# Kernel tuning notes

Measured on AMD Instinct MI355X. Metric: run time of the kernel, lower is better.

The kernel has to match this reference:

```python
import jax, jax.numpy as jnp
import numpy as np

D_MODEL = 1024
NUM_HEADS = 16
HEAD_DIM = D_MODEL // NUM_HEADS


def setup_inputs() -> dict:
    key = jax.random.key(0)
    k1, k2, k3, k4, k5 = jax.random.split(key, 5)
    s = 1.0 / np.sqrt(D_MODEL)
    return {
        "x": jax.random.normal(k1, (4, 2048, D_MODEL), dtype=jnp.float32),
        "Wqkv": jax.random.normal(k2, (D_MODEL, 3 * D_MODEL), dtype=jnp.float32) * s,
        "bqkv": jax.random.normal(k3, (3 * D_MODEL,), dtype=jnp.float32) * 0.01,
        "Wout": jax.random.normal(k4, (D_MODEL, D_MODEL), dtype=jnp.float32) * s,
        "bout": jax.random.normal(k5, (D_MODEL,), dtype=jnp.float32) * 0.01,
    }


def reference(x, Wqkv, bqkv, Wout, bout):
    B, S, _ = x.shape
    qkv = x @ Wqkv + bqkv                                   # [B, S, 3*D]
    qkv = qkv.reshape(B, S, NUM_HEADS, 3 * HEAD_DIM)
    qkv = jnp.transpose(qkv, (0, 2, 1, 3))                  # [B, H, S, 3*hd]
    q, k, v = jnp.split(qkv, 3, axis=-1)                    # each [B, H, S, hd]
    scale = 1.0 / jnp.sqrt(jnp.asarray(HEAD_DIM, dtype=x.dtype))
    scores = jnp.einsum("bhqd,bhkd->bhqk", q, k) * scale    # [B, H, S, S]
    attn = jax.nn.softmax(scores, axis=-1)
    out = jnp.einsum("bhqk,bhkd->bhqd", attn, v)            # [B, H, S, hd]
    out = jnp.transpose(out, (0, 2, 1, 3)).reshape(B, S, D_MODEL)
    return out @ Wout + bout
```

## Files before the change

### kernel.cpp

```cpp
#include <hip/hip_runtime.h>
#include <hip/hip_bf16.h>


#define S_ 2048
#define DM 1024
#define NH 16
#define HD 64

typedef unsigned short u16;
typedef unsigned int u32;
typedef __attribute__((ext_vector_type(8))) short short8;
typedef __attribute__((ext_vector_type(4))) float f32x4;
typedef __attribute__((ext_vector_type(16))) float f32x16;
typedef __attribute__((ext_vector_type(4))) u32 u32x4;

extern "C" __device__ float __ocml_native_exp2_f32(float);

#define MFMA(a, b, c) __builtin_amdgcn_mfma_f32_16x16x32_bf16((a), (b), (c), 0, 0, 0)
#define MFMA32(a, b, c) __builtin_amdgcn_mfma_f32_32x32x16_bf16((a), (b), (c), 0, 0, 0)
#define C1 0.18033688f

static __device__ __forceinline__ u16 f2bf(float f) {
  return __builtin_bit_cast(u16, __float2bfloat16(f));
}
static __device__ __forceinline__ u32 pack2bf(float a, float b) {
  return (u32)f2bf(a) | ((u32)f2bf(b) << 16);
}
static __device__ __forceinline__ short8 ld8(const u16* p) {
  return *reinterpret_cast<const short8*>(p);
}
static __device__ __forceinline__ void gl_lds16(const u16* g, u16* l) {
  __builtin_amdgcn_global_load_lds((__attribute__((address_space(1))) void*)(u16*)g,
                                   (__attribute__((address_space(3))) void*)l, 16, 0, 0);
}
static __device__ __forceinline__ void plswap(u32& a, u32& b) {
#if __has_builtin(__builtin_amdgcn_permlane32_swap)
  typedef __attribute__((ext_vector_type(2))) unsigned int u32x2_t;
  u32x2_t r = __builtin_amdgcn_permlane32_swap(a, b, false, false);
  a = r.x; b = r.y;
#else
  asm("v_permlane32_swap_b32 %0, %1" : "+v"(a), "+v"(b));
#endif
}
static __device__ __forceinline__ float xhalf_max(float x) {
  u32 a = __builtin_bit_cast(u32, x), b = a;
  plswap(a, b);
  return fmaxf(__builtin_bit_cast(float, a), __builtin_bit_cast(float, b));
}
static __device__ __forceinline__ float xhalf_sum(float x) {
  u32 a = __builtin_bit_cast(u32, x), b = a;
  plswap(a, b);
  return __builtin_bit_cast(float, a) + __builtin_bit_cast(float, b);
}

__global__ __launch_bounds__(256) void cast_x_kernel(const float4* __restrict__ in,
                                                     uint2* __restrict__ out, int n4) {
  int i = blockIdx.x * 256 + threadIdx.x;
  if (i >= n4) return;
  float4 v = in[i];
  uint2 o;
  o.x = pack2bf(v.x, v.y);
  o.y = pack2bf(v.z, v.w);
  out[i] = o;
}

__global__ __launch_bounds__(256) void transpose_cast_kernel(const float* __restrict__ in,
                                                             u16* __restrict__ out, int N) {
  __shared__ float tile[32][33];
  const int bk = blockIdx.y * 32, bn = blockIdx.x * 32;
  const int r = threadIdx.x >> 3, c4 = (threadIdx.x & 7) * 4;
  float4 v = *reinterpret_cast<const float4*>(&in[(size_t)(bk + r) * N + bn + c4]);
  tile[r][c4 + 0] = v.x; tile[r][c4 + 1] = v.y;
  tile[r][c4 + 2] = v.z; tile[r][c4 + 3] = v.w;
  __syncthreads();
  uint2 o;
  o.x = pack2bf(tile[c4 + 0][r], tile[c4 + 1][r]);
  o.y = pack2bf(tile[c4 + 2][r], tile[c4 + 3][r]);
  *reinterpret_cast<uint2*>(&out[(size_t)(bn + r) * 1024 + bk + c4]) = o;
}

__global__ __launch_bounds__(256) void gemm_bt_kernel(
    const u16* __restrict__ A, const u16* __restrict__ BT, const float* __restrict__ bias,
    int mode, u16* __restrict__ Qb, u16* __restrict__ Kb, u16* __restrict__ VT,
    float* __restrict__ outF) {
  __shared__ __align__(16) u16 As[128 * 32];
  __shared__ __align__(16) u16 Bs[128 * 32];
  const int tid = threadIdx.x, lane = tid & 63, wid = tid >> 6;
  const int m0 = blockIdx.y * 128, n0 = blockIdx.x * 128;
  const int wm = (wid >> 1) * 64, wn = (wid & 1) * 64;
  const int g = lane >> 4, lr = lane & 15;
  const int srow16 = lane >> 2, scol8 = (lane & 3) * 8;
  f32x4 acc[4][4] = {};

  for (int k0 = 0; k0 < 1024; k0 += 32) {
#pragma unroll
    for (int i = 0; i < 2; ++i) {
      int sA = wid + i * 4;
      gl_lds16(&A[(size_t)(m0 + sA * 16 + srow16) * 1024 + k0 + scol8], &As[sA * 512]);
      gl_lds16(&BT[(size_t)(n0 + sA * 16 + srow16) * 1024 + k0 + scol8], &Bs[sA * 512]);
    }
    __syncthreads();
    short8 af[4], bfr[4];
#pragma unroll
    for (int mb = 0; mb < 4; ++mb)
      af[mb] = ld8(&As[(wm + mb * 16 + lr) * 32 + g * 8]);
#pragma unroll
    for (int nb = 0; nb < 4; ++nb)
      bfr[nb] = ld8(&Bs[(wn + nb * 16 + lr) * 32 + g * 8]);
#pragma unroll
    for (int mb = 0; mb < 4; ++mb)
#pragma unroll
      for (int nb = 0; nb < 4; ++nb)
        acc[mb][nb] = MFMA(af[mb], bfr[nb], acc[mb][nb]);
    __syncthreads();
  }

  if (mode == 0) {
#pragma unroll
    for (int nb = 0; nb < 4; ++nb) {
      int col = n0 + wn + nb * 16 + lr;
      int hh = col / 192;
      int c = col - hh * 192;
      int t = c >> 6, d = c & 63;
      float bv = bias[col];
#pragma unroll
      for (int mb = 0; mb < 4; ++mb)
#pragma unroll
        for (int r = 0; r < 4; ++r) {
          int rowg = m0 + wm + mb * 16 + g * 4 + r;
          int b = rowg >> 11, s = rowg & 2047;
          u16 v = f2bf(acc[mb][nb][r] + bv);
          int head = b * NH + hh;
          if (t == 0)      Qb[(head * S_ + s) * HD + d] = v;
          else if (t == 1) Kb[(head * S_ + s) * HD + d] = v;
          else             VT[((size_t)head * HD + d) * S_ + s] = v;
        }
    }
  } else {
#pragma unroll
    for (int nb = 0; nb < 4; ++nb) {
      int col = n0 + wn + nb * 16 + lr;
      float bv = bias[col];
#pragma unroll
      for (int mb = 0; mb < 4; ++mb)
#pragma unroll
        for (int r = 0; r < 4; ++r) {
          int rowg = m0 + wm + mb * 16 + g * 4 + r;
          outF[(size_t)rowg * DM + col] = acc[mb][nb][r] + bv;
        }
    }
  }
}

__global__ __launch_bounds__(256, 2) void attn_kernel(const u16* __restrict__ Qb,
                                                      const u16* __restrict__ Kb,
                                                      const u16* __restrict__ VT,
                                                      u16* __restrict__ attn_out) {
  const int lane = threadIdx.x & 63, wid = threadIdx.x >> 6;
  const int i = blockIdx.x;
  const int head = ((i >> 7) << 3) | (i & 7);
  const int qb = (i >> 3) & 15;
  const int l31 = lane & 31, hi = lane >> 5;
  const int q = qb * 128 + wid * 32 + l31;
  const u16* Qh = Qb + (size_t)head * S_ * HD;
  const u16* Kh = Kb + (size_t)head * S_ * HD;
  const u16* Vh = VT + (size_t)head * HD * S_;

  short8 qf[4];
#pragma unroll
  for (int dt = 0; dt < 4; ++dt)
    qf[dt] = ld8(&Qh[q * HD + dt * 16 + hi * 8]);

  short8 kf[2][4];
#pragma unroll
  for (int kt = 0; kt < 2; ++kt)
#pragma unroll
    for (int dt = 0; dt < 4; ++dt)
      kf[kt][dt] = ld8(&Kh[(kt * 32 + l31) * HD + dt * 16 + hi * 8]);

  f32x16 o0 = {}, o1 = {};
  float m_run = -1e30f, l_run = 0.f;

#pragma unroll 1
  for (int kv0 = 0; kv0 < S_; kv0 += 64) {
    short8 vf0[4], vf1[4];
#pragma unroll
    for (int kc = 0; kc < 4; ++kc) {
      vf0[kc] = ld8(&Vh[(size_t)l31 * S_ + kv0 + kc * 16 + hi * 8]);
      vf1[kc] = ld8(&Vh[(size_t)(32 + l31) * S_ + kv0 + kc * 16 + hi * 8]);
    }
    f32x16 s0 = {}, s1 = {};
#pragma unroll
    for (int dt = 0; dt < 4; ++dt) s0 = MFMA32(kf[0][dt], qf[dt], s0);
#pragma unroll
    for (int dt = 0; dt < 4; ++dt) s1 = MFMA32(kf[1][dt], qf[dt], s1);
    int kvn = (kv0 + 64) & (S_ - 1);
#pragma unroll
    for (int kt = 0; kt < 2; ++kt)
#pragma unroll
      for (int dt = 0; dt < 4; ++dt)
        kf[kt][dt] = ld8(&Kh[(kvn + kt * 32 + l31) * HD + dt * 16 + hi * 8]);
    float mx[8];
#pragma unroll
    for (int r = 0; r < 8; ++r)
      mx[r] = fmaxf(fmaxf(s0[r], s0[r + 8]), fmaxf(s1[r], s1[r + 8]));
    float m01 = fmaxf(fmaxf(mx[0], mx[1]), fmaxf(mx[2], mx[3]));
    float m23 = fmaxf(fmaxf(mx[4], mx[5]), fmaxf(mx[6], mx[7]));
    float smax = xhalf_max(fmaxf(m01, m23));
    bool keep = __all(smax <= m_run + 40.0f);
    float m_new = keep ? m_run : fmaxf(m_run, smax);
    float base = m_new * C1;
    float p0 = 0.f, p1 = 0.f, p2 = 0.f, p3 = 0.f;
#pragma unroll
    for (int m = 0; m < 4; ++m) {
      s0[m * 4 + 0] = __ocml_native_exp2_f32(fmaf(s0[m * 4 + 0], C1, -base));
      s0[m * 4 + 1] = __ocml_native_exp2_f32(fmaf(s0[m * 4 + 1], C1, -base));
      s0[m * 4 + 2] = __ocml_native_exp2_f32(fmaf(s0[m * 4 + 2], C1, -base));
      s0[m * 4 + 3] = __ocml_native_exp2_f32(fmaf(s0[m * 4 + 3], C1, -base));
      s1[m * 4 + 0] = __ocml_native_exp2_f32(fmaf(s1[m * 4 + 0], C1, -base));
      s1[m * 4 + 1] = __ocml_native_exp2_f32(fmaf(s1[m * 4 + 1], C1, -base));
      s1[m * 4 + 2] = __ocml_native_exp2_f32(fmaf(s1[m * 4 + 2], C1, -base));
      s1[m * 4 + 3] = __ocml_native_exp2_f32(fmaf(s1[m * 4 + 3], C1, -base));
      p0 += s0[m * 4 + 0] + s1[m * 4 + 0];
      p1 += s0[m * 4 + 1] + s1[m * 4 + 1];
      p2 += s0[m * 4 + 2] + s1[m * 4 + 2];
      p3 += s0[m * 4 + 3] + s1[m * 4 + 3];
    }
    float psum = xhalf_sum((p0 + p1) + (p2 + p3));
    if (keep) {
      l_run += psum;
    } else {
      float corr = __ocml_native_exp2_f32((m_run - m_new) * C1);
      l_run = l_run * corr + psum;
      m_run = m_new;
#pragma unroll
      for (int r = 0; r < 16; ++r) { o0[r] *= corr; o1[r] *= corr; }
    }
    u32 wA[8], wB[8];
#pragma unroll
    for (int m = 0; m < 4; ++m) {
      wA[m] = pack2bf(s0[m * 4 + 0], s0[m * 4 + 1]);
      wB[m] = pack2bf(s0[m * 4 + 2], s0[m * 4 + 3]);
      wA[4 + m] = pack2bf(s1[m * 4 + 0], s1[m * 4 + 1]);
      wB[4 + m] = pack2bf(s1[m * 4 + 2], s1[m * 4 + 3]);
    }
#pragma unroll
    for (int kc = 0; kc < 4; ++kc) {
      u32 a0 = wA[2 * kc], a1 = wA[2 * kc + 1];
      u32 b0 = wB[2 * kc], b1 = wB[2 * kc + 1];
      plswap(a0, a1);
      plswap(b0, b1);
      u32x4 bw;
      bw.x = a0; bw.y = b0; bw.z = a1; bw.w = b1;
      short8 pf = __builtin_bit_cast(short8, bw);
      o0 = MFMA32(vf0[kc], pf, o0);
      o1 = MFMA32(vf1[kc], pf, o1);
    }
  }

  const int b = head >> 4, h = head & 15;
  float inv = 1.f / l_run;
  u16* dst = attn_out + (size_t)(b * S_ + q) * DM + h * HD;
#pragma unroll
  for (int rg = 0; rg < 4; ++rg) {
    uint2 k0, k1;
    k0.x = pack2bf(o0[rg * 4 + 0] * inv, o0[rg * 4 + 1] * inv);
    k0.y = pack2bf(o0[rg * 4 + 2] * inv, o0[rg * 4 + 3] * inv);
    *reinterpret_cast<uint2*>(dst + rg * 8 + hi * 4) = k0;
    k1.x = pack2bf(o1[rg * 4 + 0] * inv, o1[rg * 4 + 1] * inv);
    k1.y = pack2bf(o1[rg * 4 + 2] * inv, o1[rg * 4 + 3] * inv);
    *reinterpret_cast<uint2*>(dst + 32 + rg * 8 + hi * 4) = k1;
  }
}

extern "C" void kernel_launch(void* const* d_in, const int* in_sizes, int n_in,
                              void* d_out, int out_size, void* d_ws, size_t ws_size,
                              hipStream_t stream) {
  const float* x    = (const float*)d_in[0];
  const float* Wqkv = (const float*)d_in[1];
  const float* bqkv = (const float*)d_in[2];
  const float* Wout = (const float*)d_in[3];
  const float* bout = (const float*)d_in[4];
  float* out = (float*)d_out;

  char* ws = (char*)d_ws;
  u16* xb      = (u16*)(ws);
  u16* WqkvT   = (u16*)(ws + 16777216);
  u16* WoutT   = (u16*)(ws + 23068672);
  u16* Qb      = (u16*)(ws + 25165824);
  u16* Kb      = (u16*)(ws + 41943040);
  u16* VT      = (u16*)(ws + 58720256);
  u16* attn_out = xb;

  cast_x_kernel<<<8192, 256, 0, stream>>>((const float4*)x, (uint2*)xb, 8192 * 1024 / 4);
  transpose_cast_kernel<<<dim3(96, 32), 256, 0, stream>>>(Wqkv, WqkvT, 3072);
  transpose_cast_kernel<<<dim3(32, 32), 256, 0, stream>>>(Wout, WoutT, 1024);

  gemm_bt_kernel<<<dim3(24, 64), 256, 0, stream>>>(xb, WqkvT, bqkv, 0, Qb, Kb, VT, nullptr);
  attn_kernel<<<dim3(1024), 256, 0, stream>>>(Qb, Kb, VT, attn_out);
  gemm_bt_kernel<<<dim3(8, 64), 256, 0, stream>>>(attn_out, WoutT, bout, 1, nullptr, nullptr,
                                                  nullptr, out);
}
```

Before: 451.2 us.

## Split attention KV range across wave pairs and merge partial softmax via LDS

```diff
diff --git a/kernel.cpp b/kernel.cpp
--- a/kernel.cpp
+++ b/kernel.cpp
@@ -152,16 +152,19 @@
   }
 }
 
-__global__ __launch_bounds__(256, 2) void attn_kernel(const u16* __restrict__ Qb,
+__global__ __launch_bounds__(256, 8) void attn_kernel(const u16* __restrict__ Qb,
                                                       const u16* __restrict__ Kb,
                                                       const u16* __restrict__ VT,
                                                       u16* __restrict__ attn_out) {
+  __shared__ float mlds[2][64][34];
   const int lane = threadIdx.x & 63, wid = threadIdx.x >> 6;
+  const int qt = wid & 1, half = wid >> 1;
   const int i = blockIdx.x;
-  const int head = ((i >> 7) << 3) | (i & 7);
-  const int qb = (i >> 3) & 15;
+  const int head = ((i >> 8) << 3) | (i & 7);
+  const int qb = (i >> 3) & 31;
   const int l31 = lane & 31, hi = lane >> 5;
-  const int q = qb * 128 + wid * 32 + l31;
+  const int q = qb * 64 + qt * 32 + l31;
+  const int kvs = half * 1024, kve = kvs + 1024;
   const u16* Qh = Qb + (size_t)head * S_ * HD;
   const u16* Kh = Kb + (size_t)head * S_ * HD;
   const u16* Vh = VT + (size_t)head * HD * S_;
@@ -171,18 +174,17 @@
   for (int dt = 0; dt < 4; ++dt)
     qf[dt] = ld8(&Qh[q * HD + dt * 16 + hi * 8]);
 
-  short8 kf[2][4];
-#pragma unroll
-  for (int kt = 0; kt < 2; ++kt)
-#pragma unroll
-    for (int dt = 0; dt < 4; ++dt)
-      kf[kt][dt] = ld8(&Kh[(kt * 32 + l31) * HD + dt * 16 + hi * 8]);
-
   f32x16 o0 = {}, o1 = {};
   float m_run = -1e30f, l_run = 0.f;
 
 #pragma unroll 1
-  for (int kv0 = 0; kv0 < S_; kv0 += 64) {
+  for (int kv0 = kvs; kv0 < kve; kv0 += 64) {
+    short8 kf0[4], kf1[4];
+#pragma unroll
+    for (int dt = 0; dt < 4; ++dt) {
+      kf0[dt] = ld8(&Kh[(kv0 + l31) * HD + dt * 16 + hi * 8]);
+      kf1[dt] = ld8(&Kh[(kv0 + 32 + l31) * HD + dt * 16 + hi * 8]);
+    }
     short8 vf0[4], vf1[4];
 #pragma unroll
     for (int kc = 0; kc < 4; ++kc) {
@@ -191,15 +193,9 @@
     }
     f32x16 s0 = {}, s1 = {};
 #pragma unroll
-    for (int dt = 0; dt < 4; ++dt) s0 = MFMA32(kf[0][dt], qf[dt], s0);
-#pragma unroll
-    for (int dt = 0; dt < 4; ++dt) s1 = MFMA32(kf[1][dt], qf[dt], s1);
-    int kvn = (kv0 + 64) & (S_ - 1);
-#pragma unroll
-    for (int kt = 0; kt < 2; ++kt)
-#pragma unroll
-      for (int dt = 0; dt < 4; ++dt)
-        kf[kt][dt] = ld8(&Kh[(kvn + kt * 32 + l31) * HD + dt * 16 + hi * 8]);
+    for (int dt = 0; dt < 4; ++dt) s0 = MFMA32(kf0[dt], qf[dt], s0);
+#pragma unroll
+    for (int dt = 0; dt < 4; ++dt) s1 = MFMA32(kf1[dt], qf[dt], s1);
     float mx[8];
 #pragma unroll
     for (int r = 0; r < 8; ++r)
@@ -258,17 +254,37 @@
     }
   }
 
+  if (half) {
+    float* p = &mlds[qt][lane][0];
+    p[0] = m_run; p[1] = l_run;
+#pragma unroll
+    for (int r = 0; r < 16; ++r) { p[2 + r] = o0[r]; p[18 + r] = o1[r]; }
+  }
+  __syncthreads();
+  if (half) return;
+
+  const float* p = &mlds[qt][lane][0];
+  float mB = p[0], lB = p[1];
+  float m = fmaxf(m_run, mB);
+  float cA = __ocml_native_exp2_f32((m_run - m) * C1);
+  float cB = __ocml_native_exp2_f32((mB - m) * C1);
+  float inv = 1.f / (l_run * cA + lB * cB);
+  cA *= inv; cB *= inv;
+
   const int b = head >> 4, h = head & 15;
-  float inv = 1.f / l_run;
   u16* dst = attn_out + (size_t)(b * S_ + q) * DM + h * HD;
 #pragma unroll
   for (int rg = 0; rg < 4; ++rg) {
     uint2 k0, k1;
-    k0.x = pack2bf(o0[rg * 4 + 0] * inv, o0[rg * 4 + 1] * inv);
-    k0.y = pack2bf(o0[rg * 4 + 2] * inv, o0[rg * 4 + 3] * inv);
+    k0.x = pack2bf(o0[rg * 4 + 0] * cA + p[2 + rg * 4 + 0] * cB,
+                   o0[rg * 4 + 1] * cA + p[2 + rg * 4 + 1] * cB);
+    k0.y = pack2bf(o0[rg * 4 + 2] * cA + p[2 + rg * 4 + 2] * cB,
+                   o0[rg * 4 + 3] * cA + p[2 + rg * 4 + 3] * cB);
     *reinterpret_cast<uint2*>(dst + rg * 8 + hi * 4) = k0;
-    k1.x = pack2bf(o1[rg * 4 + 0] * inv, o1[rg * 4 + 1] * inv);
-    k1.y = pack2bf(o1[rg * 4 + 2] * inv, o1[rg * 4 + 3] * inv);
+    k1.x = pack2bf(o1[rg * 4 + 0] * cA + p[18 + rg * 4 + 0] * cB,
+                   o1[rg * 4 + 1] * cA + p[18 + rg * 4 + 1] * cB);
+    k1.y = pack2bf(o1[rg * 4 + 2] * cA + p[18 + rg * 4 + 2] * cB,
+                   o1[rg * 4 + 3] * cA + p[18 + rg * 4 + 3] * cB);
     *reinterpret_cast<uint2*>(dst + 32 + rg * 8 + hi * 4) = k1;
   }
 }
@@ -297,7 +313,7 @@
   transpose_cast_kernel<<<dim3(32, 32), 256, 0, stream>>>(Wout, WoutT, 1024);
 
   gemm_bt_kernel<<<dim3(24, 64), 256, 0, stream>>>(xb, WqkvT, bqkv, 0, Qb, Kb, VT, nullptr);
-  attn_kernel<<<dim3(1024), 256, 0, stream>>>(Qb, Kb, VT, attn_out);
+  attn_kernel<<<dim3(2048), 256, 0, stream>>>(Qb, Kb, VT, attn_out);
   gemm_bt_kernel<<<dim3(8, 64), 256, 0, stream>>>(attn_out, WoutT, bout, 1, nullptr, nullptr,
                                                   nullptr, out);
 }
```

Result: slower. 1.387 ms (+207.4%).
